# Optimization experiments

Hardware: AMD Instinct MI355X
Metric: run time of the kernel (lower is better)

Reference implementation:

```python
import jax, jax.numpy as jnp
import numpy as np

B, H, S, D = 4, 16, 2048, 128
D_MODEL = 128  # scale factor per module init


def setup_inputs() -> dict:
    key = jax.random.key(0)
    kq, kk, kv = jax.random.split(key, 3)
    Q = jax.random.normal(kq, (B, H, S, D), dtype=jnp.float32)
    K = jax.random.normal(kk, (B, H, S, D), dtype=jnp.float32)
    V = jax.random.normal(kv, (B, H, S, D), dtype=jnp.float32)
    return {"Q": Q, "K": K, "V": V}


def reference(Q, K, V):
    # scores: [B, H, S, S]
    scores = jnp.einsum("bhqd,bhkd->bhqk", Q, K) / np.sqrt(D_MODEL).astype(np.float32)
    # causal mask: lower-triangular keeps, upper becomes -inf
    q_idx = jnp.arange(S)[:, None]
    k_idx = jnp.arange(S)[None, :]
    causal = q_idx >= k_idx  # [S, S]
    scores = jnp.where(causal, scores, -jnp.inf)
    attn = jax.nn.softmax(scores, axis=-1)
    return jnp.einsum("bhqk,bhkd->bhqd", attn, V)
```

## Files before the change

kernel.cpp:

```cpp
#include <hip/hip_runtime.h>

typedef _Float16 f16;
typedef _Float16 f16x8 __attribute__((ext_vector_type(8)));
typedef float    f32x16 __attribute__((ext_vector_type(16)));
typedef int      i32x4 __attribute__((ext_vector_type(4)));

#define B_ 4
#define H_ 16
#define S_ 2048
#define D_ 128
#define KVB 32
#define KSTR 136
#define VTSTR 40

union U4 { i32x4 i; f16x8 h; };

__device__ __forceinline__ unsigned pk2(float a, float b) {
    auto v = __builtin_amdgcn_cvt_pkrtz(a, b);
    return __builtin_bit_cast(unsigned, v);
}

__device__ __forceinline__ f16x8 cvt8(const float4 a, const float4 b) {
    f16x8 h;
    h[0] = (f16)a.x; h[1] = (f16)a.y; h[2] = (f16)a.z; h[3] = (f16)a.w;
    h[4] = (f16)b.x; h[5] = (f16)b.y; h[6] = (f16)b.z; h[7] = (f16)b.w;
    return h;
}

__global__ __launch_bounds__(256)
void prep(const float* __restrict__ K, const float* __restrict__ V,
          f16* __restrict__ Kh, f16* __restrict__ Vtt)
{
    const int bid = blockIdx.x;
    const int bh  = bid >> 5;
    const int kb  = bid & 31;
    const int k0  = kb * 64;
    const int tid = threadIdx.x;
    const float qmul = 0.08838834764831845f * 1.4426950408889634f;

    const float* Kb = K + ((size_t)bh * S_ + k0) * D_;
    const float* Vb = V + ((size_t)bh * S_ + k0) * D_;
    f16* Khb = Kh + ((size_t)bh * S_ + k0) * D_;
    f16* Vtb = Vtt + (size_t)bh * S_ * D_ + (size_t)kb * 2 * (D_ * 32);

    #pragma unroll
    for (int it = 0; it < 4; ++it) {
        const int idx = tid + it * 256;
        const int row = idx >> 4, c8 = idx & 15;
        float4 a = *(const float4*)(Kb + row * D_ + c8 * 8);
        float4 b = *(const float4*)(Kb + row * D_ + c8 * 8 + 4);
        a.x *= qmul; a.y *= qmul; a.z *= qmul; a.w *= qmul;
        b.x *= qmul; b.y *= qmul; b.z *= qmul; b.w *= qmul;
        *(f16x8*)(Khb + row * D_ + c8 * 8) = cvt8(a, b);
    }
    #pragma unroll
    for (int it = 0; it < 4; ++it) {
        const int idx = tid + it * 256;
        const int d  = idx & 127;
        const int k8 = idx >> 7;
        const int t  = k8 >> 2;
        const int o  = k8 & 3;
        const int c  = o >> 1, odd = o & 1;
        const int kbase = t * 32 + c * 16 + odd * 4;
        const float* vp0 = Vb + (size_t)kbase * D_ + d;
        const float* vp1 = vp0 + (size_t)8 * D_;
        f16x8 vh;
        #pragma unroll
        for (int e = 0; e < 4; ++e) vh[e] = (f16)vp0[(size_t)e * D_];
        #pragma unroll
        for (int e = 0; e < 4; ++e) vh[4 + e] = (f16)vp1[(size_t)e * D_];
        *(f16x8*)(Vtb + (size_t)t * (D_ * 32) + d * 32 + o * 8) = vh;
    }
}

__device__ __constant__ int QTA[11] = {15, 14, 13, 12, 11, 10, 9, 8, 7, 6, 5};
__device__ __constant__ int QTB[11] = {-1, -1, -1, -1, -1, -1, 0, 1, 2, 3, 4};

__global__ __launch_bounds__(256, 3)
void fattn18(const float* __restrict__ Qg, const f16* __restrict__ Khg,
             const f16* __restrict__ Vttg, float* __restrict__ Og)
{
    __shared__ __align__(16) f16 Klds[2][KVB * KSTR];
    __shared__ __align__(16) f16 Vl[2][128 * VTSTR];

    const int id  = blockIdx.x;
    const int xcd = id & 7;
    const int r   = id >> 3;
    const int bh  = xcd + 8 * (r & 7);
    const int bin = r >> 3;

    const int tid  = threadIdx.x;
    const int lane = tid & 63;
    const int l31  = lane & 31;
    const int h    = lane >> 5;
    const int wv   = tid >> 6;

    const float* Qb  = Qg   + (size_t)bh * S_ * D_;
    const f16*   Khb = Khg  + (size_t)bh * S_ * D_;
    const f16*   Vtb = Vttg + (size_t)bh * S_ * D_;
    float*       Ob  = Og   + (size_t)bh * S_ * D_;

    const f16* kS = Khb + (tid >> 4) * D_ + (tid & 15) * 8;
    const f16* vS = Vtb + (size_t)tid * 8;
    const int  kDo = (tid >> 4) * KSTR + (tid & 15) * 8;
    const int  vDo = (tid >> 2) * VTSTR + (tid & 3) * 8;

    i32x4 kr[2], vr[2];
    auto issue = [&](int kt) {
        const f16* kp = kS + ((size_t)kt << 12);
        const f16* vp = vS + ((size_t)kt << 12);
        kr[0] = *(const i32x4*)kp;
        kr[1] = *(const i32x4*)(kp + 2048);
        vr[0] = *(const i32x4*)vp;
        vr[1] = *(const i32x4*)(vp + 2048);
    };
    auto writeLds = [&](int buf) {
        f16* kb = &Klds[buf][0];
        f16* vb = &Vl[buf][0];
        *(i32x4*)(kb + kDo)              = kr[0];
        *(i32x4*)(kb + kDo + 16 * KSTR)  = kr[1];
        *(i32x4*)(vb + vDo)              = vr[0];
        *(i32x4*)(vb + vDo + 64 * VTSTR) = vr[1];
    };

    const int nph = (QTB[bin] >= 0) ? 2 : 1;

    #pragma unroll 1
    for (int ph = 0; ph < nph; ++ph) {
        const int qt  = ph ? QTB[bin] : QTA[bin];
        const int qw0 = qt * 128 + wv * 32;
        const int qg  = qw0 + l31;
        const int nkt = 4 * qt + 4;
        const int lastt = 4 * qt + wv;

        f16x8 qf[8];
        {
            const float* Qrow = Qb + (size_t)(qw0 + l31) * D_;
            #pragma unroll
            for (int dc = 0; dc < 8; ++dc) {
                const float4 a = *(const float4*)(Qrow + dc * 16 + h * 8);
                const float4 b = *(const float4*)(Qrow + dc * 16 + h * 8 + 4);
                qf[dc] = cvt8(a, b);
            }
        }

        f32x16 acc[4];
        #pragma unroll
        for (int dt = 0; dt < 4; ++dt)
            #pragma unroll
            for (int q = 0; q < 16; ++q) acc[dt][q] = 0.f;
        float m_i = -1e30f, l_i = 0.f;

        __syncthreads();
        issue(0);
        writeLds(0);
        if (nkt > 1) issue(1);
        __syncthreads();

        for (int kt = 0; kt < nkt; ++kt) {
            const int cur = kt & 1;

            if (kt <= lastt) {
                const int k0 = kt * KVB;
                f32x16 sv;
                #pragma unroll
                for (int q = 0; q < 16; ++q) sv[q] = 0.f;
                __builtin_amdgcn_s_setprio(1);
                #pragma unroll
                for (int dc = 0; dc < 8; ++dc) {
                    const f16x8 kf = *(const f16x8*)&Klds[cur][l31 * KSTR + dc * 16 + h * 8];
                    sv = __builtin_amdgcn_mfma_f32_32x32x16_f16(kf, qf[dc], sv, 0, 0, 0);
                }
                __builtin_amdgcn_s_setprio(0);
                if (k0 + 31 > qw0) {
                    #pragma unroll
                    for (int q = 0; q < 16; ++q) {
                        const int kg = k0 + (q & 3) + 8 * (q >> 2) + 4 * h;
                        if (kg > qg) sv[q] = -1e30f;
                    }
                }
                const float a1 = fmaxf(fmaxf(sv[0], sv[1]), sv[2]);
                const float a2 = fmaxf(fmaxf(sv[3], sv[4]), sv[5]);
                const float a3 = fmaxf(fmaxf(sv[6], sv[7]), sv[8]);
                const float a4 = fmaxf(fmaxf(sv[9], sv[10]), sv[11]);
                const float a5 = fmaxf(fmaxf(sv[12], sv[13]), sv[14]);
                float mx = fmaxf(fmaxf(a1, a2), a3);
                mx = fmaxf(fmaxf(mx, a4), a5);
                mx = fmaxf(mx, sv[15]);
                mx = fmaxf(mx, __shfl_xor(mx, 32));
                if (!__all(mx - m_i <= 8.0f)) {
                    const float mn = fmaxf(m_i, mx);
                    const float al = exp2f(m_i - mn);
                    m_i = mn;
                    l_i *= al;
                    float arow[16];
                    #pragma unroll
                    for (int q = 0; q < 16; ++q)
                        arow[q] = __shfl(al, (q & 3) + 8 * (q >> 2) + 4 * h);
                    #pragma unroll
                    for (int dt = 0; dt < 4; ++dt)
                        #pragma unroll
                        for (int q = 0; q < 16; ++q) acc[dt][q] *= arow[q];
                }
                #pragma unroll
                for (int q = 0; q < 16; ++q) sv[q] = exp2f(sv[q] - m_i);
                float s8[8];
                #pragma unroll
                for (int q = 0; q < 8; ++q) s8[q] = sv[2 * q] + sv[2 * q + 1];
                #pragma unroll
                for (int q = 0; q < 4; ++q) s8[q] += s8[q + 4];
                s8[0] += s8[2]; s8[1] += s8[3];
                float rsum = s8[0] + s8[1];
                rsum += __shfl_xor(rsum, 32);
                l_i += rsum;
                U4 pa0, pa1;
                #pragma unroll
                for (int m = 0; m < 4; ++m) {
                    pa0.i[m] = (int)pk2(sv[2 * m],     sv[2 * m + 1]);
                    pa1.i[m] = (int)pk2(sv[8 + 2 * m], sv[9 + 2 * m]);
                }
                __builtin_amdgcn_s_setprio(1);
                #pragma unroll
                for (int dt = 0; dt < 4; ++dt) {
                    const f16* vrow = &Vl[cur][(dt * 32 + l31) * VTSTR + h * 8];
                    const f16x8 b0 = *(const f16x8*)(vrow + 0);
                    const f16x8 b1 = *(const f16x8*)(vrow + 16);
                    acc[dt] = __builtin_amdgcn_mfma_f32_32x32x16_f16(pa0.h, b0, acc[dt], 0, 0, 0);
                    acc[dt] = __builtin_amdgcn_mfma_f32_32x32x16_f16(pa1.h, b1, acc[dt], 0, 0, 0);
                }
                __builtin_amdgcn_s_setprio(0);
            }

            if (kt + 1 < nkt) {
                writeLds(cur ^ 1);
                if (kt + 2 < nkt) issue(kt + 2);
                __syncthreads();
            }
        }

        float li[16];
        #pragma unroll
        for (int q = 0; q < 16; ++q) {
            const float lv = __shfl(l_i, (q & 3) + 8 * (q >> 2) + 4 * h);
            li[q] = 1.0f / lv;
        }
        #pragma unroll
        for (int dt = 0; dt < 4; ++dt)
            #pragma unroll
            for (int q = 0; q < 16; ++q) {
                const int row = qw0 + (q & 3) + 8 * (q >> 2) + 4 * h;
                Ob[(size_t)row * D_ + dt * 32 + l31] = acc[dt][q] * li[q];
            }
    }
}

__global__ __launch_bounds__(256, 3)
void fattn5(const float* __restrict__ Qg, const float* __restrict__ Kg,
            const float* __restrict__ Vg, float* __restrict__ Og)
{
    __shared__ __align__(16) f16 Klds[2][KVB * KSTR];
    __shared__ __align__(16) f16 Vt[2][128 * VTSTR];
    const int id  = blockIdx.x;
    const int xcd = id & 7;
    const int w   = id >> 3;
    const int qt  = 15 - (w & 15);
    const int bh  = xcd + 8 * (w >> 4);
    const int tid  = threadIdx.x;
    const int lane = tid & 63;
    const int wv   = tid >> 6;
    const int l31  = lane & 31;
    const int h    = lane >> 5;
    const int qw0 = qt * 128 + wv * 32;
    const int qg  = qw0 + l31;
    const size_t base = (size_t)bh * S_ * D_;
    const float* Qb = Qg + base;
    const float* Kb = Kg + base;
    const float* Vb = Vg + base;
    float*       Ob = Og + base;
    const int nkt = 4 * qt + 4;
    float4 kr[4];
    float  vr[16];
    auto issue = [&](int kt) {
        const int k0n = kt * KVB;
        #pragma unroll
        for (int it = 0; it < 2; ++it) {
            const int idx  = tid + it * 256;
            const int krow = idx >> 4;
            const int c8   = idx & 15;
            const float* kp = Kb + (size_t)(k0n + krow) * D_ + c8 * 8;
            kr[it * 2]     = *(const float4*)kp;
            kr[it * 2 + 1] = *(const float4*)(kp + 4);
            const int d  = idx & 127;
            const int k8 = idx >> 7;
            const float* vp = Vb + (size_t)(k0n + k8 * 8) * D_ + d;
            #pragma unroll
            for (int e = 0; e < 8; ++e) vr[it * 8 + e] = vp[(size_t)e * D_];
        }
    };
    auto writeLds = [&](int buf) {
        #pragma unroll
        for (int it = 0; it < 2; ++it) {
            const int idx  = tid + it * 256;
            const int krow = idx >> 4;
            const int c8   = idx & 15;
            *(f16x8*)&Klds[buf][krow * KSTR + c8 * 8] = cvt8(kr[it * 2], kr[it * 2 + 1]);
            const int d  = idx & 127;
            const int k8 = idx >> 7;
            f16x8 vh;
            #pragma unroll
            for (int e = 0; e < 8; ++e) vh[e] = (f16)vr[it * 8 + e];
            *(f16x8*)&Vt[buf][d * VTSTR + k8 * 8] = vh;
        }
    };
    const float qmul = 0.08838834764831845f * 1.4426950408889634f;
    f16x8 qf[8];
    {
        const float* Qrow = Qb + (size_t)(qw0 + l31) * D_;
        #pragma unroll
        for (int dc = 0; dc < 8; ++dc) {
            const float4 a = *(const float4*)(Qrow + dc * 16 + h * 8);
            const float4 b = *(const float4*)(Qrow + dc * 16 + h * 8 + 4);
            f16x8 q;
            q[0] = (f16)(a.x * qmul); q[1] = (f16)(a.y * qmul);
            q[2] = (f16)(a.z * qmul); q[3] = (f16)(a.w * qmul);
            q[4] = (f16)(b.x * qmul); q[5] = (f16)(b.y * qmul);
            q[6] = (f16)(b.z * qmul); q[7] = (f16)(b.w * qmul);
            qf[dc] = q;
        }
    }
    f32x16 acc[4];
    #pragma unroll
    for (int dt = 0; dt < 4; ++dt)
        #pragma unroll
        for (int q = 0; q < 16; ++q) acc[dt][q] = 0.f;
    float m_i = -1e30f, l_i = 0.f;
    issue(0);
    writeLds(0);
    if (nkt > 1) issue(1);
    __syncthreads();
    for (int kt = 0; kt < nkt; ++kt) {
        const int k0  = kt * KVB;
        const int cur = kt & 1;
        if (k0 <= qw0 + 31) {
            f32x16 sv;
            #pragma unroll
            for (int q = 0; q < 16; ++q) sv[q] = 0.f;
            #pragma unroll
            for (int dc = 0; dc < 8; ++dc) {
                const f16x8 kf = *(const f16x8*)&Klds[cur][l31 * KSTR + dc * 16 + h * 8];
                sv = __builtin_amdgcn_mfma_f32_32x32x16_f16(kf, qf[dc], sv, 0, 0, 0);
            }
            if (k0 + 31 > qw0) {
                #pragma unroll
                for (int q = 0; q < 16; ++q) {
                    const int kg = k0 + (q & 3) + 8 * (q >> 2) + 4 * h;
                    if (kg > qg) sv[q] = -1e30f;
                }
            }
            float mx = sv[0];
            #pragma unroll
            for (int q = 1; q < 16; ++q) mx = fmaxf(mx, sv[q]);
            mx = fmaxf(mx, __shfl_xor(mx, 32));
            if (!__all(mx - m_i <= 8.0f)) {
                const float mn = fmaxf(m_i, mx);
                const float al = exp2f(m_i - mn);
                m_i = mn;
                l_i *= al;
                float arow[16];
                #pragma unroll
                for (int q = 0; q < 16; ++q)
                    arow[q] = __shfl(al, (q & 3) + 8 * (q >> 2) + 4 * h);
                #pragma unroll
                for (int dt = 0; dt < 4; ++dt)
                    #pragma unroll
                    for (int q = 0; q < 16; ++q) acc[dt][q] *= arow[q];
            }
            float rsum = 0.f;
            #pragma unroll
            for (int q = 0; q < 16; ++q) {
                sv[q] = exp2f(sv[q] - m_i);
                rsum += sv[q];
            }
            rsum += __shfl_xor(rsum, 32);
            l_i += rsum;
            U4 pa[2];
            {
                unsigned dwp[8];
                #pragma unroll
                for (int m = 0; m < 8; ++m) dwp[m] = pk2(sv[2 * m], sv[2 * m + 1]);
                #pragma unroll
                for (int hf = 0; hf < 2; ++hf) {
                    const unsigned a0 = dwp[hf * 4 + 0], a1 = dwp[hf * 4 + 1];
                    const unsigned b0 = dwp[hf * 4 + 2], b1 = dwp[hf * 4 + 3];
                    const unsigned sa0 = (unsigned)__shfl_xor((int)a0, 32);
                    const unsigned sa1 = (unsigned)__shfl_xor((int)a1, 32);
                    const unsigned sb0 = (unsigned)__shfl_xor((int)b0, 32);
                    const unsigned sb1 = (unsigned)__shfl_xor((int)b1, 32);
                    i32x4 d;
                    d[0] = h ? (int)sb0 : (int)a0;
                    d[1] = h ? (int)sb1 : (int)a1;
                    d[2] = h ? (int)b0  : (int)sa0;
                    d[3] = h ? (int)b1  : (int)sa1;
                    pa[hf].i = d;
                }
            }
            #pragma unroll
            for (int dt = 0; dt < 4; ++dt) {
                const f16* vrow = &Vt[cur][(dt * 32 + l31) * VTSTR + h * 8];
                const f16x8 vb0 = *(const f16x8*)(vrow + 0);
                const f16x8 vb1 = *(const f16x8*)(vrow + 16);
                acc[dt] = __builtin_amdgcn_mfma_f32_32x32x16_f16(pa[0].h, vb0, acc[dt], 0, 0, 0);
                acc[dt] = __builtin_amdgcn_mfma_f32_32x32x16_f16(pa[1].h, vb1, acc[dt], 0, 0, 0);
            }
        }
        if (kt + 1 < nkt) {
            writeLds(cur ^ 1);
            if (kt + 2 < nkt) issue(kt + 2);
            __syncthreads();
        }
    }
    float li[16];
    #pragma unroll
    for (int q = 0; q < 16; ++q) {
        const float lv = __shfl(l_i, (q & 3) + 8 * (q >> 2) + 4 * h);
        li[q] = 1.0f / lv;
    }
    #pragma unroll
    for (int dt = 0; dt < 4; ++dt)
        #pragma unroll
        for (int q = 0; q < 16; ++q) {
            const int row = qw0 + (q & 3) + 8 * (q >> 2) + 4 * h;
            Ob[(size_t)row * D_ + dt * 32 + l31] = acc[dt][q] * li[q];
        }
}

extern "C" void kernel_launch(void* const* d_in, const int* in_sizes, int n_in,
                              void* d_out, int out_size, void* d_ws, size_t ws_size,
                              hipStream_t stream) {
    (void)in_sizes; (void)n_in; (void)out_size;
    const float* Q = (const float*)d_in[0];
    const float* K = (const float*)d_in[1];
    const float* V = (const float*)d_in[2];
    float* O = (float*)d_out;
    const size_t elems  = (size_t)B_ * H_ * S_ * D_;
    const size_t needKV = elems * 2 * sizeof(f16);
    if (ws_size >= needKV) {
        f16* Kh  = (f16*)d_ws;
        f16* Vtt = Kh + elems;
        prep<<<dim3(B_ * H_ * (S_ / 64)), dim3(256), 0, stream>>>(K, V, Kh, Vtt);
        fattn18<<<dim3(704), dim3(256), 0, stream>>>(Q, Kh, Vtt, O);
    } else {
        fattn5<<<dim3((S_ / 128) * B_ * H_), dim3(256), 0, stream>>>(Q, K, V, O);
    }
}
```

Measured before the change: 163.6 us.

## Software-pipeline QK^T one tile ahead with triple-buffered LDS and paired q-tiles

The attention kernel now computes the next tile's QK^T scores while the current tile's softmax and PV MFMAs run, using three LDS buffers for K/V instead of two. The q-tile schedule changes from a constant-table bin layout (704 blocks) to symmetric pairs (p, 15-p), giving 512 blocks that each do equal causal work. Launch bounds drop to 2 blocks per SM to make room for the extra registers and LDS. The aim is to hide MFMA latency and balance load, at the cost of occupancy and register pressure.

```diff
diff --git a/kernel.cpp b/kernel.cpp
--- a/kernel.cpp
+++ b/kernel.cpp
@@ -73,21 +73,18 @@
     }
 }
 
-__device__ __constant__ int QTA[11] = {15, 14, 13, 12, 11, 10, 9, 8, 7, 6, 5};
-__device__ __constant__ int QTB[11] = {-1, -1, -1, -1, -1, -1, 0, 1, 2, 3, 4};
-
-__global__ __launch_bounds__(256, 3)
-void fattn18(const float* __restrict__ Qg, const f16* __restrict__ Khg,
+__global__ __launch_bounds__(256, 2)
+void fattn20(const float* __restrict__ Qg, const f16* __restrict__ Khg,
              const f16* __restrict__ Vttg, float* __restrict__ Og)
 {
-    __shared__ __align__(16) f16 Klds[2][KVB * KSTR];
-    __shared__ __align__(16) f16 Vl[2][128 * VTSTR];
+    __shared__ __align__(16) f16 Klds[3][KVB * KSTR];
+    __shared__ __align__(16) f16 Vt[3][128 * VTSTR];
 
     const int id  = blockIdx.x;
     const int xcd = id & 7;
     const int r   = id >> 3;
     const int bh  = xcd + 8 * (r & 7);
-    const int bin = r >> 3;
+    const int p   = r >> 3;
 
     const int tid  = threadIdx.x;
     const int lane = tid & 63;
@@ -116,24 +113,45 @@
     };
     auto writeLds = [&](int buf) {
         f16* kb = &Klds[buf][0];
-        f16* vb = &Vl[buf][0];
+        f16* vb = &Vt[buf][0];
         *(i32x4*)(kb + kDo)              = kr[0];
         *(i32x4*)(kb + kDo + 16 * KSTR)  = kr[1];
         *(i32x4*)(vb + vDo)              = vr[0];
         *(i32x4*)(vb + vDo + 64 * VTSTR) = vr[1];
     };
-
-    const int nph = (QTB[bin] >= 0) ? 2 : 1;
+    f16x8 qf[8];
+    auto qkt = [&](int buf) {
+        const f16* base = &Klds[buf][l31 * KSTR + h * 8];
+        f16x8 kf0 = *(const f16x8*)(base + 0 * 16);
+        f16x8 kf1 = *(const f16x8*)(base + 1 * 16);
+        f16x8 kf2 = *(const f16x8*)(base + 2 * 16);
+        f16x8 kf3 = *(const f16x8*)(base + 3 * 16);
+        f16x8 kf4 = *(const f16x8*)(base + 4 * 16);
+        f16x8 kf5 = *(const f16x8*)(base + 5 * 16);
+        f16x8 kf6 = *(const f16x8*)(base + 6 * 16);
+        f16x8 kf7 = *(const f16x8*)(base + 7 * 16);
+        f32x16 a;
+        #pragma unroll
+        for (int q = 0; q < 16; ++q) a[q] = 0.f;
+        a = __builtin_amdgcn_mfma_f32_32x32x16_f16(kf0, qf[0], a, 0, 0, 0);
+        a = __builtin_amdgcn_mfma_f32_32x32x16_f16(kf1, qf[1], a, 0, 0, 0);
+        a = __builtin_amdgcn_mfma_f32_32x32x16_f16(kf2, qf[2], a, 0, 0, 0);
+        a = __builtin_amdgcn_mfma_f32_32x32x16_f16(kf3, qf[3], a, 0, 0, 0);
+        a = __builtin_amdgcn_mfma_f32_32x32x16_f16(kf4, qf[4], a, 0, 0, 0);
+        a = __builtin_amdgcn_mfma_f32_32x32x16_f16(kf5, qf[5], a, 0, 0, 0);
+        a = __builtin_amdgcn_mfma_f32_32x32x16_f16(kf6, qf[6], a, 0, 0, 0);
+        a = __builtin_amdgcn_mfma_f32_32x32x16_f16(kf7, qf[7], a, 0, 0, 0);
+        return a;
+    };
 
     #pragma unroll 1
-    for (int ph = 0; ph < nph; ++ph) {
-        const int qt  = ph ? QTB[bin] : QTA[bin];
+    for (int ph = 0; ph < 2; ++ph) {
+        const int qt  = ph ? 15 - p : p;
         const int qw0 = qt * 128 + wv * 32;
         const int qg  = qw0 + l31;
         const int nkt = 4 * qt + 4;
         const int lastt = 4 * qt + wv;
 
-        f16x8 qf[8];
         {
             const float* Qrow = Qb + (size_t)(qw0 + l31) * D_;
             #pragma unroll
@@ -152,26 +170,26 @@
         float m_i = -1e30f, l_i = 0.f;
 
         __syncthreads();
-        issue(0);
-        writeLds(0);
-        if (nkt > 1) issue(1);
+        issue(0);  writeLds(0);
+        issue(1);  writeLds(1);
+        if (nkt > 2) issue(2);
         __syncthreads();
-
+        f32x16 sv = qkt(0);
+
+        int bB = 0, bA = 1, bW = 2;
         for (int kt = 0; kt < nkt; ++kt) {
-            const int cur = kt & 1;
+            __syncthreads();
+            if (kt + 2 < nkt) {
+                writeLds(bW);
+                if (kt + 3 < nkt) issue(kt + 3);
+            }
+
+            __builtin_amdgcn_s_setprio(1);
+            f32x16 svn;
+            if (kt + 1 < nkt && kt + 1 <= lastt) svn = qkt(bA);
 
             if (kt <= lastt) {
                 const int k0 = kt * KVB;
-                f32x16 sv;
-                #pragma unroll
-                for (int q = 0; q < 16; ++q) sv[q] = 0.f;
-                __builtin_amdgcn_s_setprio(1);
-                #pragma unroll
-                for (int dc = 0; dc < 8; ++dc) {
-                    const f16x8 kf = *(const f16x8*)&Klds[cur][l31 * KSTR + dc * 16 + h * 8];
-                    sv = __builtin_amdgcn_mfma_f32_32x32x16_f16(kf, qf[dc], sv, 0, 0, 0);
-                }
-                __builtin_amdgcn_s_setprio(0);
                 if (k0 + 31 > qw0) {
                     #pragma unroll
                     for (int q = 0; q < 16; ++q) {
@@ -179,13 +197,13 @@
                         if (kg > qg) sv[q] = -1e30f;
                     }
                 }
-                const float a1 = fmaxf(fmaxf(sv[0], sv[1]), sv[2]);
-                const float a2 = fmaxf(fmaxf(sv[3], sv[4]), sv[5]);
-                const float a3 = fmaxf(fmaxf(sv[6], sv[7]), sv[8]);
-                const float a4 = fmaxf(fmaxf(sv[9], sv[10]), sv[11]);
-                const float a5 = fmaxf(fmaxf(sv[12], sv[13]), sv[14]);
-                float mx = fmaxf(fmaxf(a1, a2), a3);
-                mx = fmaxf(fmaxf(mx, a4), a5);
+                const float m1 = fmaxf(fmaxf(sv[0], sv[1]), sv[2]);
+                const float m2 = fmaxf(fmaxf(sv[3], sv[4]), sv[5]);
+                const float m3 = fmaxf(fmaxf(sv[6], sv[7]), sv[8]);
+                const float m4 = fmaxf(fmaxf(sv[9], sv[10]), sv[11]);
+                const float m5 = fmaxf(fmaxf(sv[12], sv[13]), sv[14]);
+                float mx = fmaxf(fmaxf(m1, m2), m3);
+                mx = fmaxf(fmaxf(mx, m4), m5);
                 mx = fmaxf(mx, sv[15]);
                 mx = fmaxf(mx, __shfl_xor(mx, 32));
                 if (!__all(mx - m_i <= 8.0f)) {
@@ -219,23 +237,28 @@
                     pa0.i[m] = (int)pk2(sv[2 * m],     sv[2 * m + 1]);
                     pa1.i[m] = (int)pk2(sv[8 + 2 * m], sv[9 + 2 * m]);
                 }
-                __builtin_amdgcn_s_setprio(1);
-                #pragma unroll
-                for (int dt = 0; dt < 4; ++dt) {
-                    const f16* vrow = &Vl[cur][(dt * 32 + l31) * VTSTR + h * 8];
-                    const f16x8 b0 = *(const f16x8*)(vrow + 0);
-                    const f16x8 b1 = *(const f16x8*)(vrow + 16);
-                    acc[dt] = __builtin_amdgcn_mfma_f32_32x32x16_f16(pa0.h, b0, acc[dt], 0, 0, 0);
-                    acc[dt] = __builtin_amdgcn_mfma_f32_32x32x16_f16(pa1.h, b1, acc[dt], 0, 0, 0);
-                }
-                __builtin_amdgcn_s_setprio(0);
-            }
-
-            if (kt + 1 < nkt) {
-                writeLds(cur ^ 1);
-                if (kt + 2 < nkt) issue(kt + 2);
-                __syncthreads();
-            }
+                const f16* vbase = &Vt[bB][l31 * VTSTR + h * 8];
+                f16x8 vb0 = *(const f16x8*)(vbase + 0 * 32 * VTSTR);
+                f16x8 vb1 = *(const f16x8*)(vbase + 0 * 32 * VTSTR + 16);
+                f16x8 vb2 = *(const f16x8*)(vbase + 1 * 32 * VTSTR);
+                f16x8 vb3 = *(const f16x8*)(vbase + 1 * 32 * VTSTR + 16);
+                f16x8 vb4 = *(const f16x8*)(vbase + 2 * 32 * VTSTR);
+                f16x8 vb5 = *(const f16x8*)(vbase + 2 * 32 * VTSTR + 16);
+                f16x8 vb6 = *(const f16x8*)(vbase + 3 * 32 * VTSTR);
+                f16x8 vb7 = *(const f16x8*)(vbase + 3 * 32 * VTSTR + 16);
+                acc[0] = __builtin_amdgcn_mfma_f32_32x32x16_f16(pa0.h, vb0, acc[0], 0, 0, 0);
+                acc[0] = __builtin_amdgcn_mfma_f32_32x32x16_f16(pa1.h, vb1, acc[0], 0, 0, 0);
+                acc[1] = __builtin_amdgcn_mfma_f32_32x32x16_f16(pa0.h, vb2, acc[1], 0, 0, 0);
+                acc[1] = __builtin_amdgcn_mfma_f32_32x32x16_f16(pa1.h, vb3, acc[1], 0, 0, 0);
+                acc[2] = __builtin_amdgcn_mfma_f32_32x32x16_f16(pa0.h, vb4, acc[2], 0, 0, 0);
+                acc[2] = __builtin_amdgcn_mfma_f32_32x32x16_f16(pa1.h, vb5, acc[2], 0, 0, 0);
+                acc[3] = __builtin_amdgcn_mfma_f32_32x32x16_f16(pa0.h, vb6, acc[3], 0, 0, 0);
+                acc[3] = __builtin_amdgcn_mfma_f32_32x32x16_f16(pa1.h, vb7, acc[3], 0, 0, 0);
+            }
+            __builtin_amdgcn_s_setprio(0);
+
+            if (kt + 1 < nkt) sv = svn;
+            const int t = bB; bB = bA; bA = bW; bW = t;
         }
 
         float li[16];
@@ -448,7 +471,7 @@
         f16* Kh  = (f16*)d_ws;
         f16* Vtt = Kh + elems;
         prep<<<dim3(B_ * H_ * (S_ / 64)), dim3(256), 0, stream>>>(K, V, Kh, Vtt);
-        fattn18<<<dim3(704), dim3(256), 0, stream>>>(Q, Kh, Vtt, O);
+        fattn20<<<dim3(512), dim3(256), 0, stream>>>(Q, Kh, Vtt, O);
     } else {
         fattn5<<<dim3((S_ / 128) * B_ * H_), dim3(256), 0, stream>>>(Q, K, V, O);
     }
```

Result: faster. 154.7 us, median of 2 (-5.4%).
